# Kernel tuning notes

Measured on AMD Instinct MI355X. Metric: run time of the kernel, lower is better.

The kernel has to match this reference:

```python
import jax, jax.numpy as jnp
import numpy as np

B = 64
NUM_ENT = 40000
NUM_REL = 1345
DIM = 200
N_LIT = 100


def setup_inputs() -> dict:
    key = jax.random.key(0)
    ks = jax.random.split(key, 8)
    e1_idx = jax.random.randint(ks[0], (B,), 0, NUM_ENT)
    r_idx = jax.random.randint(ks[1], (B,), 0, NUM_REL)
    E_weight = jax.random.normal(ks[2], (NUM_ENT, DIM), dtype=jnp.float32) * 0.1
    R_weight = jax.random.normal(ks[3], (NUM_REL, DIM), dtype=jnp.float32) * 0.1
    # numerical literals are min-max normalized to [0, 1]
    num_lit = jax.random.uniform(ks[4], (NUM_ENT, N_LIT), dtype=jnp.float32)
    c = jax.random.normal(ks[5], (N_LIT,), dtype=jnp.float32) * 0.1
    var = jax.random.uniform(ks[6], (N_LIT,), dtype=jnp.float32) * 0.1 + 1e-3  # positive
    nf_weights = jax.random.normal(ks[7], (NUM_REL, N_LIT), dtype=jnp.float32) * 0.1
    return {"e1_idx": e1_idx, "r_idx": r_idx, "E_weight": E_weight,
            "R_weight": R_weight, "num_lit": num_lit, "c": c, "var": var,
            "nf_weights": nf_weights}


def reference(e1_idx, r_idx, E_weight, R_weight, num_lit, c, var, nf_weights):
    # Dropout is identity in eval mode.
    e1 = E_weight[e1_idx]                      # [B, D]
    r = R_weight[r_idx]                        # [B, D]
    score_l = jnp.einsum('bd,ed->be', e1 * r, E_weight)   # [B, E]

    n_h = num_lit[e1_idx]                      # [B, L]
    # broadcast instead of repeat: [B, 1, L] - [1, E, L] -> [B, E, L]
    n = n_h[:, None, :] - num_lit[None, :, :]
    phi = jnp.exp(-((n - c) ** 2) / var)       # RBF, [B, E, L]
    w_nf = nf_weights[r_idx]                   # [B, L]
    score_n = jnp.einsum('bel,bl->be', phi, w_nf)          # [B, E]

    return jax.nn.sigmoid(score_l + score_n)
```

## Files before the change

kernel.cpp:

```cpp
#include <hip/hip_runtime.h>

#define NB 64
#define NE 40000
#define DIM 200
#define NL 100
#define EBLK 32
#define NTHREADS 256
#define D4 50
#define L4 25
#define LOG2E 1.4426950408889634f

#define WS_E1R 0

typedef float f32x4 __attribute__((ext_vector_type(4)));
typedef short bf16x8 __attribute__((ext_vector_type(8)));

__device__ __forceinline__ unsigned int f2bf(float f) {
    unsigned int u = __float_as_uint(f);
    return (u + 0x7fffu + ((u >> 16) & 1u)) >> 16;
}
__device__ __forceinline__ unsigned int packbf(float a, float b) {
    return f2bf(a) | (f2bf(b) << 16);
}

__global__ void DistMult_prep_kernel(
    const int* __restrict__ e1_idx, const int* __restrict__ r_idx,
    const float* __restrict__ Ew, const float* __restrict__ Rw,
    unsigned char* __restrict__ ws)
{
    const int t = blockIdx.x * NTHREADS + threadIdx.x;
    unsigned int* e1r = (unsigned int*)(ws + WS_E1R);
    const float4* E4 = (const float4*)Ew;
    const float4* R4 = (const float4*)Rw;

    for (int f = t; f < NB * 28; f += 8 * NTHREADS) {
        int b = f / 28, c = f % 28;
        uint4 st = {0u, 0u, 0u, 0u};
        if (c < 25) {
            float4 a0 = E4[(size_t)e1_idx[b] * D4 + 2 * c];
            float4 a1 = E4[(size_t)e1_idx[b] * D4 + 2 * c + 1];
            float4 r0 = R4[(size_t)r_idx[b] * D4 + 2 * c];
            float4 r1 = R4[(size_t)r_idx[b] * D4 + 2 * c + 1];
            st.x = packbf(a0.x * r0.x, a0.y * r0.y);
            st.y = packbf(a0.z * r0.z, a0.w * r0.w);
            st.z = packbf(a1.x * r1.x, a1.y * r1.y);
            st.w = packbf(a1.z * r1.z, a1.w * r1.w);
        }
        *(uint4*)(e1r + (size_t)b * 112 + c * 4) = st;
    }
}

union SMem {
    struct {
        unsigned short A[NB * 128];
        unsigned short Bm[EBLK * 128];
    } p1;
    struct {
        float xsT[28][32];
        float asT[28][64];
        float wT[28][64];
    } p2;
    float scat[NB * 33];
};

__global__ __launch_bounds__(NTHREADS, 5)
void DistMult_KBLN_79164837200204_kernel(
    const int* __restrict__ e1_idx, const int* __restrict__ r_idx,
    const float* __restrict__ Ew, const float* __restrict__ num_lit,
    const float* __restrict__ cvec, const float* __restrict__ var,
    const float* __restrict__ nfw,
    const unsigned char* __restrict__ ws, float* __restrict__ out)
{
    __shared__ SMem sm;
    __shared__ float sS[NL];
    __shared__ int sIdxE[NB], sIdxR[NB];

    const int t = threadIdx.x;
    const int nq = (NE / EBLK) >> 3, nr = (NE / EBLK) & 7;
    const int xcd = blockIdx.x & 7, sub = blockIdx.x >> 3;
    const int wg = (xcd < nr ? xcd * (nq + 1) : nr * (nq + 1) + (xcd - nr) * nq) + sub;
    const int e0 = wg * EBLK;

    const int L = t & 63, w = t >> 6;
    const int l15 = L & 15, lq = L >> 4;

    if (t < NL) sS[t] = sqrtf(LOG2E / var[t]);
    if (t < NB) { sIdxE[t] = e1_idx[t]; sIdxR[t] = r_idx[t]; }

    unsigned short* pA = (unsigned short*)sm.p1.A;
    unsigned short* pB = (unsigned short*)sm.p1.Bm;
    for (int i = t; i < 1024; i += NTHREADS) ((unsigned int*)pA)[i] = 0u;
    for (int i = t; i < 512;  i += NTHREADS) ((unsigned int*)pB)[i] = 0u;
    __syncthreads();
    if (t < 64) {
        pA[t * 32]     = (unsigned short)f2bf(256.0f * t);
        pA[t * 32 + 1] = (unsigned short)f2bf(1.0f);
    } else if (t < 96) {
        int e = t - 64;
        pB[e * 32]     = (unsigned short)f2bf(1.0f);
        pB[e * 32 + 1] = (unsigned short)f2bf((float)e);
    }
    __syncthreads();
    int ib0[4], ib1[4];
    {
        bf16x8 afp = *(const bf16x8*)(pA + (16 * w + l15) * 32 + lq * 8);
        bf16x8 b0p = *(const bf16x8*)(pB + l15 * 32 + lq * 8);
        bf16x8 b1p = *(const bf16x8*)(pB + (16 + l15) * 32 + lq * 8);
        f32x4 z = {0.f, 0.f, 0.f, 0.f};
        f32x4 p0 = __builtin_amdgcn_mfma_f32_16x16x32_bf16(afp, b0p, z, 0, 0, 0);
        f32x4 p1 = __builtin_amdgcn_mfma_f32_16x16x32_bf16(afp, b1p, z, 0, 0, 0);
        #pragma unroll
        for (int r = 0; r < 4; ++r) { ib0[r] = (int)p0[r]; ib1[r] = (int)p1[r]; }
    }
    __syncthreads();

    f32x4 acc0 = {0.f, 0.f, 0.f, 0.f};
    f32x4 acc1 = {0.f, 0.f, 0.f, 0.f};

    const float4* E4 = (const float4*)Ew;
    const uint4* wsA = (const uint4*)(ws + WS_E1R);

    #pragma unroll
    for (int h = 0; h < 2; ++h) {
        const int nc = h ? 12 : 16;
        for (int f = t; f < NB * nc; f += NTHREADS) {
            int b = f / nc, c = f % nc;
            uint4 v = wsA[(size_t)b * 28 + h * 16 + c];
            int off = (b * 256 + c * 16) ^ ((b & 7) << 4);
            *(uint4*)((char*)sm.p1.A + off) = v;
        }
        for (int f = t; f < EBLK * nc; f += NTHREADS) {
            int e = f / nc, c = f % nc;
            int dg = h * 128 + c * 8;
            uint4 st = {0u, 0u, 0u, 0u};
            if (dg <= DIM - 8) {
                float4 v0 = E4[(size_t)(e0 + e) * D4 + (dg >> 2)];
                float4 v1 = E4[(size_t)(e0 + e) * D4 + (dg >> 2) + 1];
                st.x = packbf(v0.x, v0.y);
                st.y = packbf(v0.z, v0.w);
                st.z = packbf(v1.x, v1.y);
                st.w = packbf(v1.z, v1.w);
            }
            int off = (e * 256 + c * 16) ^ ((e & 7) << 4);
            *(uint4*)((char*)sm.p1.Bm + off) = st;
        }
        __syncthreads();

        const int nst = h ? 3 : 4;
        const int arow = 16 * w + l15;
        const int aswz = (arow & 7) << 4;
        const int bswz = (l15 & 7) << 4;
        #pragma unroll
        for (int s = 0; s < 4; ++s) {
            if (s < nst) {
                int kb = s * 64 + lq * 16;
                bf16x8 af = *(const bf16x8*)((const char*)sm.p1.A + ((arow * 256 + kb) ^ aswz));
                bf16x8 b0 = *(const bf16x8*)((const char*)sm.p1.Bm + ((l15 * 256 + kb) ^ bswz));
                bf16x8 b1 = *(const bf16x8*)((const char*)sm.p1.Bm + (((16 + l15) * 256 + kb) ^ bswz));
                acc0 = __builtin_amdgcn_mfma_f32_16x16x32_bf16(af, b0, acc0, 0, 0, 0);
                acc1 = __builtin_amdgcn_mfma_f32_16x16x32_bf16(af, b1, acc1, 0, 0, 0);
            }
        }
        __syncthreads();
    }

    #pragma unroll
    for (int r = 0; r < 4; ++r) {
        sm.scat[(ib0[r] >> 8) * 33 + (ib0[r] & 255)] = acc0[r];
        sm.scat[(ib1[r] >> 8) * 33 + (ib1[r] & 255)] = acc1[r];
    }
    __syncthreads();

    const int tx = t & 7;
    const int ty = t >> 3;
    float2 acc2[4];
    #pragma unroll
    for (int j = 0; j < 4; ++j) {
        acc2[j].x = sm.scat[(2 * ty) * 33 + 4 * tx + j];
        acc2[j].y = sm.scat[(2 * ty + 1) * 33 + 4 * tx + j];
    }
    __syncthreads();

    const float4* N4 = (const float4*)num_lit;
    const float4* C4 = (const float4*)cvec;
    const float4* W4 = (const float4*)nfw;

    #pragma unroll
    for (int q = 0; q < 4; ++q) {
        const int ol  = q * 28;
        const int ol4 = q * 7;
        const int nl4 = (q < 3) ? 7 : 4;
        for (int f = t; f < EBLK * nl4; f += NTHREADS) {
            int e = f & 31;
            int l4 = f >> 5;
            float4 v = N4[(e0 + e) * 25 + ol4 + l4];
            int lg = ol + 4 * l4;
            sm.p2.xsT[4 * l4 + 0][e] = v.x * sS[lg + 0];
            sm.p2.xsT[4 * l4 + 1][e] = v.y * sS[lg + 1];
            sm.p2.xsT[4 * l4 + 2][e] = v.z * sS[lg + 2];
            sm.p2.xsT[4 * l4 + 3][e] = v.w * sS[lg + 3];
        }
        for (int f = t; f < NB * nl4; f += NTHREADS) {
            int b = f & 63;
            int l4 = f >> 6;
            float4 v = N4[sIdxE[b] * 25 + ol4 + l4];
            float4 cc = C4[ol4 + l4];
            int lg = ol + 4 * l4;
            sm.p2.asT[4 * l4 + 0][b] = (v.x - cc.x) * sS[lg + 0];
            sm.p2.asT[4 * l4 + 1][b] = (v.y - cc.y) * sS[lg + 1];
            sm.p2.asT[4 * l4 + 2][b] = (v.z - cc.z) * sS[lg + 2];
            sm.p2.asT[4 * l4 + 3][b] = (v.w - cc.w) * sS[lg + 3];
        }
        for (int f = t; f < NB * nl4; f += NTHREADS) {
            int b = f & 63;
            int l4 = f >> 6;
            float4 v = W4[sIdxR[b] * 25 + ol4 + l4];
            sm.p2.wT[4 * l4 + 0][b] = v.x;
            sm.p2.wT[4 * l4 + 1][b] = v.y;
            sm.p2.wT[4 * l4 + 2][b] = v.z;
            sm.p2.wT[4 * l4 + 3][b] = v.w;
        }
        __syncthreads();

        const int nl = 4 * nl4;
        #pragma unroll 4
        for (int l = 0; l < nl; ++l) {
            float4 xs = *(const float4*)&sm.p2.xsT[l][4 * tx];
            float2 as = *(const float2*)&sm.p2.asT[l][2 * ty];
            float2 w2 = *(const float2*)&sm.p2.wT[l][2 * ty];
            float xj[4] = { xs.x, xs.y, xs.z, xs.w };
            #pragma unroll
            for (int j = 0; j < 4; ++j) {
                float m0 = as.x - xj[j];
                float m1 = as.y - xj[j];
                float p0 = __builtin_amdgcn_exp2f(-(m0 * m0));
                float p1 = __builtin_amdgcn_exp2f(-(m1 * m1));
                acc2[j].x = fmaf(p0, w2.x, acc2[j].x);
                acc2[j].y = fmaf(p1, w2.y, acc2[j].y);
            }
        }
        __syncthreads();
    }

    {
        float4 o0, o1;
        float* p0 = (float*)&o0;
        float* p1 = (float*)&o1;
        #pragma unroll
        for (int j = 0; j < 4; ++j) {
            float ex0 = __builtin_amdgcn_exp2f(-LOG2E * acc2[j].x);
            float ex1 = __builtin_amdgcn_exp2f(-LOG2E * acc2[j].y);
            p0[j] = __builtin_amdgcn_rcpf(1.0f + ex0);
            p1[j] = __builtin_amdgcn_rcpf(1.0f + ex1);
        }
        size_t b0 = 2 * ty;
        *(float4*)&out[b0 * NE + e0 + 4 * tx] = o0;
        *(float4*)&out[(b0 + 1) * NE + e0 + 4 * tx] = o1;
    }
}

extern "C" void kernel_launch(void* const* d_in, const int* in_sizes, int n_in,
                              void* d_out, int out_size, void* d_ws, size_t ws_size,
                              hipStream_t stream) {
    const int*   e1_idx  = (const int*)d_in[0];
    const int*   r_idx   = (const int*)d_in[1];
    const float* Ew      = (const float*)d_in[2];
    const float* Rw      = (const float*)d_in[3];
    const float* num_lit = (const float*)d_in[4];
    const float* cvec    = (const float*)d_in[5];
    const float* var     = (const float*)d_in[6];
    const float* nfw     = (const float*)d_in[7];
    float* out = (float*)d_out;

    DistMult_prep_kernel<<<8, NTHREADS, 0, stream>>>(
        e1_idx, r_idx, Ew, Rw, (unsigned char*)d_ws);
    DistMult_KBLN_79164837200204_kernel<<<NE / EBLK, NTHREADS, 0, stream>>>(
        e1_idx, r_idx, Ew, num_lit, cvec, var, nfw,
        (const unsigned char*)d_ws, out);
}
```

Measured before the change: 60.49 us.

## Prefetch per-wave RBF operands into registers and drop block barriers in literal loop

Replaces the SMem union with explicit byte offsets. All 100 literal columns of the entity tile are now staged once, rather than in four chunks. The query-side (n_h - c)*s and weight values are interleaved into a per-wave float4 layout, and the next chunk is prefetched into registers while the current chunk computes. Each wave then writes its own slice, so the per-chunk __syncthreads become wave-local waitcnt fences, which removes block-wide barriers and the redundant global loads. The costs are extra registers, a larger shared footprint, and reliance on wave-local ordering being correct.

```diff
diff --git a/kernel.cpp b/kernel.cpp
--- a/kernel.cpp
+++ b/kernel.cpp
@@ -11,6 +11,13 @@
 #define LOG2E 1.4426950408889634f
 
 #define WS_E1R 0
+
+#define A_OFF    0
+#define BM_OFF   16384
+#define SCAT_OFF 0
+#define XS_OFF   0
+#define ASW_OFF  12800
+#define SMEM_BYTES 27136
 
 typedef float f32x4 __attribute__((ext_vector_type(4)));
 typedef short bf16x8 __attribute__((ext_vector_type(8)));
@@ -50,18 +57,44 @@
     }
 }
 
-union SMem {
-    struct {
-        unsigned short A[NB * 128];
-        unsigned short Bm[EBLK * 128];
-    } p1;
-    struct {
-        float xsT[28][32];
-        float asT[28][64];
-        float wT[28][64];
-    } p2;
-    float scat[NB * 33];
-};
+__device__ __forceinline__ bool asw_load(
+    const float4* N4, const float4* C4, const float4* W4,
+    const int* sIdxE, const int* sIdxR, int w, int L, int ol4, int nl4,
+    float4& n0, float4& n1, float4& cc, float4& w0, float4& w1,
+    int& pc4, int& pi0)
+{
+    pc4 = L & 7; pi0 = L >> 3;
+    if (pc4 >= nl4) return false;
+    int b0 = 16 * w + pi0, b1 = b0 + 8;
+    n0 = N4[(size_t)sIdxE[b0] * L4 + ol4 + pc4];
+    n1 = N4[(size_t)sIdxE[b1] * L4 + ol4 + pc4];
+    cc = C4[ol4 + pc4];
+    w0 = W4[(size_t)sIdxR[b0] * L4 + ol4 + pc4];
+    w1 = W4[(size_t)sIdxR[b1] * L4 + ol4 + pc4];
+    return true;
+}
+
+__device__ __forceinline__ void asw_write(
+    float* aswW, const float* sS, int olq, int pc4, int pi0,
+    const float4& n0, const float4& n1, const float4& cc,
+    const float4& w0, const float4& w1)
+{
+    const float* n0f = (const float*)&n0;
+    const float* n1f = (const float*)&n1;
+    const float* ccf = (const float*)&cc;
+    const float* w0f = (const float*)&w0;
+    const float* w1f = (const float*)&w1;
+    const int p0 = pi0 >> 1, h0 = pi0 & 1;
+    #pragma unroll
+    for (int k = 0; k < 4; ++k) {
+        int l = 4 * pc4 + k;
+        float s = sS[olq + l];
+        float2 v0; v0.x = (n0f[k] - ccf[k]) * s; v0.y = w0f[k];
+        float2 v1; v1.x = (n1f[k] - ccf[k]) * s; v1.y = w1f[k];
+        *(float2*)(aswW + (l * 8 + p0) * 4 + h0 * 2) = v0;
+        *(float2*)(aswW + (l * 8 + p0 + 4) * 4 + h0 * 2) = v1;
+    }
+}
 
 __global__ __launch_bounds__(NTHREADS, 5)
 void DistMult_KBLN_79164837200204_kernel(
@@ -71,7 +104,7 @@
     const float* __restrict__ nfw,
     const unsigned char* __restrict__ ws, float* __restrict__ out)
 {
-    __shared__ SMem sm;
+    __shared__ __align__(16) char smem[SMEM_BYTES];
     __shared__ float sS[NL];
     __shared__ int sIdxE[NB], sIdxR[NB];
 
@@ -83,29 +116,30 @@
 
     const int L = t & 63, w = t >> 6;
     const int l15 = L & 15, lq = L >> 4;
+    const int tx = t & 7, ty = t >> 3, tyl = L >> 3;
 
     if (t < NL) sS[t] = sqrtf(LOG2E / var[t]);
     if (t < NB) { sIdxE[t] = e1_idx[t]; sIdxR[t] = r_idx[t]; }
 
-    unsigned short* pA = (unsigned short*)sm.p1.A;
-    unsigned short* pB = (unsigned short*)sm.p1.Bm;
+    unsigned short* pA  = (unsigned short*)(smem + A_OFF);
+    unsigned short* pBm = (unsigned short*)(smem + BM_OFF);
     for (int i = t; i < 1024; i += NTHREADS) ((unsigned int*)pA)[i] = 0u;
-    for (int i = t; i < 512;  i += NTHREADS) ((unsigned int*)pB)[i] = 0u;
+    for (int i = t; i < 512;  i += NTHREADS) ((unsigned int*)pBm)[i] = 0u;
     __syncthreads();
     if (t < 64) {
         pA[t * 32]     = (unsigned short)f2bf(256.0f * t);
         pA[t * 32 + 1] = (unsigned short)f2bf(1.0f);
     } else if (t < 96) {
         int e = t - 64;
-        pB[e * 32]     = (unsigned short)f2bf(1.0f);
-        pB[e * 32 + 1] = (unsigned short)f2bf((float)e);
+        pBm[e * 32]     = (unsigned short)f2bf(1.0f);
+        pBm[e * 32 + 1] = (unsigned short)f2bf((float)e);
     }
     __syncthreads();
     int ib0[4], ib1[4];
     {
         bf16x8 afp = *(const bf16x8*)(pA + (16 * w + l15) * 32 + lq * 8);
-        bf16x8 b0p = *(const bf16x8*)(pB + l15 * 32 + lq * 8);
-        bf16x8 b1p = *(const bf16x8*)(pB + (16 + l15) * 32 + lq * 8);
+        bf16x8 b0p = *(const bf16x8*)(pBm + l15 * 32 + lq * 8);
+        bf16x8 b1p = *(const bf16x8*)(pBm + (16 + l15) * 32 + lq * 8);
         f32x4 z = {0.f, 0.f, 0.f, 0.f};
         f32x4 p0 = __builtin_amdgcn_mfma_f32_16x16x32_bf16(afp, b0p, z, 0, 0, 0);
         f32x4 p1 = __builtin_amdgcn_mfma_f32_16x16x32_bf16(afp, b1p, z, 0, 0, 0);
@@ -127,7 +161,7 @@
             int b = f / nc, c = f % nc;
             uint4 v = wsA[(size_t)b * 28 + h * 16 + c];
             int off = (b * 256 + c * 16) ^ ((b & 7) << 4);
-            *(uint4*)((char*)sm.p1.A + off) = v;
+            *(uint4*)(smem + A_OFF + off) = v;
         }
         for (int f = t; f < EBLK * nc; f += NTHREADS) {
             int e = f / nc, c = f % nc;
@@ -142,7 +176,7 @@
                 st.w = packbf(v1.z, v1.w);
             }
             int off = (e * 256 + c * 16) ^ ((e & 7) << 4);
-            *(uint4*)((char*)sm.p1.Bm + off) = st;
+            *(uint4*)(smem + BM_OFF + off) = st;
         }
         __syncthreads();
 
@@ -154,9 +188,9 @@
         for (int s = 0; s < 4; ++s) {
             if (s < nst) {
                 int kb = s * 64 + lq * 16;
-                bf16x8 af = *(const bf16x8*)((const char*)sm.p1.A + ((arow * 256 + kb) ^ aswz));
-                bf16x8 b0 = *(const bf16x8*)((const char*)sm.p1.Bm + ((l15 * 256 + kb) ^ bswz));
-                bf16x8 b1 = *(const bf16x8*)((const char*)sm.p1.Bm + (((16 + l15) * 256 + kb) ^ bswz));
+                bf16x8 af = *(const bf16x8*)(smem + A_OFF + ((arow * 256 + kb) ^ aswz));
+                bf16x8 b0 = *(const bf16x8*)(smem + BM_OFF + ((l15 * 256 + kb) ^ bswz));
+                bf16x8 b1 = *(const bf16x8*)(smem + BM_OFF + (((16 + l15) * 256 + kb) ^ bswz));
                 acc0 = __builtin_amdgcn_mfma_f32_16x16x32_bf16(af, b0, acc0, 0, 0, 0);
                 acc1 = __builtin_amdgcn_mfma_f32_16x16x32_bf16(af, b1, acc1, 0, 0, 0);
             }
@@ -164,82 +198,73 @@
         __syncthreads();
     }
 
+    float* scat = (float*)(smem + SCAT_OFF);
     #pragma unroll
     for (int r = 0; r < 4; ++r) {
-        sm.scat[(ib0[r] >> 8) * 33 + (ib0[r] & 255)] = acc0[r];
-        sm.scat[(ib1[r] >> 8) * 33 + (ib1[r] & 255)] = acc1[r];
-    }
-    __syncthreads();
-
-    const int tx = t & 7;
-    const int ty = t >> 3;
+        scat[(ib0[r] >> 8) * 33 + (ib0[r] & 255)] = acc0[r];
+        scat[(ib1[r] >> 8) * 33 + (ib1[r] & 255)] = acc1[r];
+    }
+    __syncthreads();
+
     float2 acc2[4];
     #pragma unroll
     for (int j = 0; j < 4; ++j) {
-        acc2[j].x = sm.scat[(2 * ty) * 33 + 4 * tx + j];
-        acc2[j].y = sm.scat[(2 * ty + 1) * 33 + 4 * tx + j];
+        acc2[j].x = scat[(2 * ty) * 33 + 4 * tx + j];
+        acc2[j].y = scat[(2 * ty + 1) * 33 + 4 * tx + j];
     }
     __syncthreads();
 
     const float4* N4 = (const float4*)num_lit;
     const float4* C4 = (const float4*)cvec;
     const float4* W4 = (const float4*)nfw;
+    float* xsF  = (float*)(smem + XS_OFF);
+    float* aswW = (float*)(smem + ASW_OFF) + w * 896;
+
+    float4 n0, n1, ccv, wv0, wv1; int pc4, pi0;
+    bool pv = asw_load(N4, C4, W4, sIdxE, sIdxR, w, L, 0, 7,
+                       n0, n1, ccv, wv0, wv1, pc4, pi0);
+    for (int f = t; f < 32 * 32; f += NTHREADS) {
+        int e = f >> 5, c4s = f & 31;
+        if (c4s < L4) {
+            float4 v = N4[(size_t)(e0 + e) * L4 + c4s];
+            const float* vf = (const float*)&v;
+            #pragma unroll
+            for (int k = 0; k < 4; ++k)
+                xsF[(4 * c4s + k) * 32 + e] = vf[k] * sS[4 * c4s + k];
+        }
+    }
+    if (pv) asw_write(aswW, sS, 0, pc4, pi0, n0, n1, ccv, wv0, wv1);
+    __syncthreads();
 
     #pragma unroll
     for (int q = 0; q < 4; ++q) {
-        const int ol  = q * 28;
-        const int ol4 = q * 7;
-        const int nl4 = (q < 3) ? 7 : 4;
-        for (int f = t; f < EBLK * nl4; f += NTHREADS) {
-            int e = f & 31;
-            int l4 = f >> 5;
-            float4 v = N4[(e0 + e) * 25 + ol4 + l4];
-            int lg = ol + 4 * l4;
-            sm.p2.xsT[4 * l4 + 0][e] = v.x * sS[lg + 0];
-            sm.p2.xsT[4 * l4 + 1][e] = v.y * sS[lg + 1];
-            sm.p2.xsT[4 * l4 + 2][e] = v.z * sS[lg + 2];
-            sm.p2.xsT[4 * l4 + 3][e] = v.w * sS[lg + 3];
-        }
-        for (int f = t; f < NB * nl4; f += NTHREADS) {
-            int b = f & 63;
-            int l4 = f >> 6;
-            float4 v = N4[sIdxE[b] * 25 + ol4 + l4];
-            float4 cc = C4[ol4 + l4];
-            int lg = ol + 4 * l4;
-            sm.p2.asT[4 * l4 + 0][b] = (v.x - cc.x) * sS[lg + 0];
-            sm.p2.asT[4 * l4 + 1][b] = (v.y - cc.y) * sS[lg + 1];
-            sm.p2.asT[4 * l4 + 2][b] = (v.z - cc.z) * sS[lg + 2];
-            sm.p2.asT[4 * l4 + 3][b] = (v.w - cc.w) * sS[lg + 3];
-        }
-        for (int f = t; f < NB * nl4; f += NTHREADS) {
-            int b = f & 63;
-            int l4 = f >> 6;
-            float4 v = W4[sIdxR[b] * 25 + ol4 + l4];
-            sm.p2.wT[4 * l4 + 0][b] = v.x;
-            sm.p2.wT[4 * l4 + 1][b] = v.y;
-            sm.p2.wT[4 * l4 + 2][b] = v.z;
-            sm.p2.wT[4 * l4 + 3][b] = v.w;
-        }
-        __syncthreads();
-
-        const int nl = 4 * nl4;
+        const int nl = (q < 3) ? 28 : 16;
+        const int ol = q * 28;
+        if (q < 3)
+            pv = asw_load(N4, C4, W4, sIdxE, sIdxR, w, L,
+                          (q + 1) * 7, (q + 1 < 3) ? 7 : 4,
+                          n0, n1, ccv, wv0, wv1, pc4, pi0);
         #pragma unroll 4
         for (int l = 0; l < nl; ++l) {
-            float4 xs = *(const float4*)&sm.p2.xsT[l][4 * tx];
-            float2 as = *(const float2*)&sm.p2.asT[l][2 * ty];
-            float2 w2 = *(const float2*)&sm.p2.wT[l][2 * ty];
+            float4 xs = *(const float4*)(xsF + (ol + l) * 32 + 4 * tx);
+            float4 aw = *(const float4*)(aswW + (l * 8 + tyl) * 4);
             float xj[4] = { xs.x, xs.y, xs.z, xs.w };
             #pragma unroll
             for (int j = 0; j < 4; ++j) {
-                float m0 = as.x - xj[j];
-                float m1 = as.y - xj[j];
+                float m0 = aw.x - xj[j];
+                float m1 = aw.z - xj[j];
                 float p0 = __builtin_amdgcn_exp2f(-(m0 * m0));
                 float p1 = __builtin_amdgcn_exp2f(-(m1 * m1));
-                acc2[j].x = fmaf(p0, w2.x, acc2[j].x);
-                acc2[j].y = fmaf(p1, w2.y, acc2[j].y);
+                acc2[j].x = fmaf(p0, aw.y, acc2[j].x);
+                acc2[j].y = fmaf(p1, aw.w, acc2[j].y);
             }
         }
-        __syncthreads();
+        if (q < 3) {
+            asm volatile("s_waitcnt lgkmcnt(0)" ::: "memory");
+            if (pv) asw_write(aswW, sS, (q + 1) * 28, pc4, pi0,
+                              n0, n1, ccv, wv0, wv1);
+            asm volatile("s_waitcnt lgkmcnt(0)" ::: "memory");
+        }
     }
 
     {
```

New measurement: 64.93 us. 7.4% more time.
